# Performance work log

Hardware: AMD Instinct MI355X
Metric: run time of the kernel (lower is better)

Reference implementation:

```python
import jax, jax.numpy as jnp
import numpy as np

L_IN, L_K = 1, 1            # degree ranges (0..L)
C_IN, K_CH, H = 16, 8, 4    # in_channels, k_channels (per head), num_heads
C_OUT = H * K_CH            # 32
E, N_NODES, EMB = 32768, 4096, 64
M_IN, M_K = (L_IN + 1) ** 2, (L_K + 1) ** 2


def _so2_pairs(L_in, L_out):
    # enumerate SO(2)-equivariant weight blocks: for each order m, all (l_in, l_out)
    # pairs with l >= m; m=0 uses 1 matrix, m>0 uses 2 (real/imag parts).
    pairs, w = [], 0
    for m in range(min(L_in, L_out) + 1):
        for l_in in range(m, L_in + 1):
            for l_out in range(m, L_out + 1):
                pairs.append((m, l_in, l_out, w))
                w += 1 if m == 0 else 2
    return pairs, w

_PAIRS, NUM_W = _so2_pairs(L_IN, L_K)  # NUM_W = 6 for L_in=L_k=1


def so2_linear(x, W, L_in, L_out):
    # x: [E, (L_in+1)^2, Cin]; W: [NUM_W, Cin, Cout] (shared) or [E, NUM_W, Cin, Cout] (per-edge)
    per_edge = (W.ndim == 4)
    Cout = W.shape[-1]
    out = jnp.zeros((x.shape[0], (L_out + 1) ** 2, Cout), x.dtype)

    def mat(xs, w):
        return jnp.einsum('ec,eco->eo', xs, W[:, w]) if per_edge else xs @ W[w]

    pairs, _ = _so2_pairs(L_in, L_out)
    for m, l_in, l_out, w in pairs:
        i_in, i_out = l_in * (l_in + 1), l_out * (l_out + 1)  # flat index of (l, m=0)
        if m == 0:
            out = out.at[:, i_out].add(mat(x[:, i_in], w))
        else:
            xp, xn = x[:, i_in + m], x[:, i_in - m]
            out = out.at[:, i_out + m].add(mat(xp, w) - mat(xn, w + 1))
            out = out.at[:, i_out - m].add(mat(xp, w + 1) + mat(xn, w))
    return out


def segment_softmax(z, index, num_segments):
    # PyG-style softmax over ragged neighborhoods (max is detached, as in PyG)
    zmax = jax.lax.stop_gradient(jax.ops.segment_max(z, index, num_segments=num_segments))
    e = jnp.exp(z - zmax[index])
    denom = jax.ops.segment_sum(e, index, num_segments=num_segments)
    return e / denom[index]


def setup_inputs() -> dict:
    key = jax.random.key(0)
    ks = jax.random.split(key, 6)
    x_q = jax.random.normal(ks[0], (E, M_IN, C_IN), jnp.float32)
    x_k = jax.random.normal(ks[1], (E, M_IN, C_IN), jnp.float32)
    edge_emb = jax.random.normal(ks[2], (E, EMB), jnp.float32)
    index = jnp.sort(jax.random.randint(ks[3], (E,), 0, N_NODES))
    W_q = jax.random.normal(ks[4], (NUM_W, C_IN, C_OUT), jnp.float32) / np.sqrt(C_IN)
    W_p = jax.random.normal(ks[5], (EMB, NUM_W * C_IN * C_OUT), jnp.float32) / np.sqrt(EMB)
    return {"x_q": x_q, "x_k": x_k, "edge_emb": edge_emb, "index": index,
            "W_q": W_q, "W_p": W_p, "num_nodes": N_NODES}


def reference(x_q, x_k, edge_emb, index, W_q, W_p, num_nodes):
    # q_ij = W_Q x_i ; static SO2 weights
    q = so2_linear(x_q, W_q, L_IN, L_K).reshape(-1, M_K, H, K_CH)
    # k_ij = W_K(||r_ij||) x_j ; per-edge dynamic SO2 weights from edge embedding
    W_k = (edge_emb @ W_p).reshape(-1, NUM_W, C_IN, C_OUT)
    k = so2_linear(x_k, W_k, L_IN, L_K).reshape(-1, M_K, H, K_CH)
    scale = (K_CH // H) ** (-0.5)  # faithful to original: (k_channels // num_heads)**-0.5
    z = (q * k).sum((-1, -3)) * scale  # [E, H]
    return segment_softmax(z, index, num_nodes)
```

## Files before the change

kernel.cpp:

```cpp
#include <hip/hip_runtime.h>
#include <math.h>

#define E_TOTAL 32768
#define NUM_NODES 4096
#define SCALE 0.70710678118654752f

typedef __attribute__((ext_vector_type(8))) short bfrag;
typedef __attribute__((ext_vector_type(16))) float facc;

#define MFMA __builtin_amdgcn_mfma_f32_32x32x16_bf16

__device__ inline unsigned short f2bf(float f) {
  unsigned int u = __float_as_uint(f);
  unsigned int r = (u + 0x7FFFu + ((u >> 16) & 1u)) >> 16;
  return (unsigned short)r;
}
__device__ inline float bf2f(unsigned short s) {
  return __uint_as_float(((unsigned int)s) << 16);
}
__device__ inline void cvt8(const float* v, bfrag& hi, bfrag& lo) {
#pragma unroll
  for (int i = 0; i < 8; ++i) {
    unsigned short h = f2bf(v[i]);
    hi[i] = (short)h;
    lo[i] = (short)f2bf(v[i] - bf2f(h));
  }
}

__global__ __launch_bounds__(256) void prep_kernel(
    const float* __restrict__ Wp, const float* __restrict__ Wq,
    const int* __restrict__ index,
    unsigned short* __restrict__ fragWp, unsigned short* __restrict__ fragWq,
    int* __restrict__ offs)
{
  const int b = blockIdx.x, t = threadIdx.x;
  if (b < 96) {
    __shared__ unsigned short lds[4096];
    const int c = b / 6, w = b - c * 6;
    const int colbase = w * 512 + c * 32;
    const int cl = t & 31, dg = t >> 5;
#pragma unroll
    for (int i = 0; i < 8; ++i) {
      const int d = dg * 8 + i;
      const float v = Wp[(size_t)d * 3072 + colbase + cl];
      const unsigned short hi = f2bf(v);
      const unsigned short lo = f2bf(v - bf2f(hi));
      const int ks = d >> 4;
      const int lane = ((d >> 3) & 1) * 32 + cl;
      const int j = d & 7;
      lds[(ks * 2 + 0) * 512 + lane * 8 + j] = hi;
      lds[(ks * 2 + 1) * 512 + lane * 8 + j] = lo;
    }
    __syncthreads();
    const int wslot0 = (w == 0) ? 0 : (w == 1) ? 64 : (w == 2) ? 16
                     : (w == 3) ? 80 : (w == 4) ? 32 : 48;
    unsigned short* dst = fragWp + (size_t)(wslot0 + c) * 4096;
    ((uint4*)dst)[t] = ((const uint4*)lds)[t];
    ((uint4*)dst)[t + 256] = ((const uint4*)lds)[t + 256];
  } else if (b < 103) {
    const int slot = b - 96;
    const int w = (slot == 6) ? 5 : slot;
    const float sgn = (slot == 6) ? -1.f : 1.f;
    for (int tt = t; tt < 512; tt += 256) {
      const int lane = tt >> 3, j = tt & 7;
      const int o = lane & 31, c = (lane >> 5) * 8 + j;
      const float v = sgn * Wq[(size_t)(w * 16 + c) * 32 + o];
      const unsigned short hi = f2bf(v);
      const unsigned short lo = f2bf(v - bf2f(hi));
      fragWq[slot * 1024 + lane * 8 + j] = hi;
      fragWq[slot * 1024 + 512 + lane * 8 + j] = lo;
    }
  } else {
    const int tg = (b - 103) * 256 + t;
    if (tg >= E_TOTAL) return;
    const int cur = index[tg];
    const int prev = (tg == 0) ? -1 : index[tg - 1];
    for (int n = prev + 1; n <= cur; ++n) offs[n] = tg;
    if (tg == E_TOTAL - 1)
      for (int n = cur + 1; n <= NUM_NODES; ++n) offs[n] = E_TOTAL;
  }
}

__global__ __launch_bounds__(256, 1) void main_kernel(
    const float* __restrict__ x_q, const float* __restrict__ x_k,
    const float* __restrict__ emb,
    const unsigned short* __restrict__ fragWp,
    const unsigned short* __restrict__ fragWq,
    float* __restrict__ z)
{
  __shared__ float xk_t[64][129];
  __shared__ float zred[4][64][4];

  const int t = threadIdx.x;
  const int lane = t & 63, wv = t >> 6;
  const int pr = wv & 1, pairI = wv >> 1;
  const int col = lane & 31, half = lane >> 5;
  const int eb = blockIdx.x * 128;
  const int el0 = pairI * 64 + col;
  const int el1 = el0 + 32;
  const int e0 = eb + el0, e1 = eb + el1;

  {
    const int er = t & 127, dh = (t >> 7) * 32;
    const float* src = x_k + (size_t)(eb + er) * 64 + dh;
#pragma unroll
    for (int i = 0; i < 8; ++i) {
      float4 v = *(const float4*)(src + i * 4);
      xk_t[dh + i * 4 + 0][er] = v.x;
      xk_t[dh + i * 4 + 1][er] = v.y;
      xk_t[dh + i * 4 + 2][er] = v.z;
      xk_t[dh + i * 4 + 3][er] = v.w;
    }
  }

  bfrag ebh0[4], ebl0[4], ebh1[4], ebl1[4];
#pragma unroll
  for (int ks = 0; ks < 4; ++ks) {
    float tmp[8];
    *(float4*)&tmp[0] = *(const float4*)(emb + (size_t)e0 * 64 + ks * 16 + half * 8);
    *(float4*)&tmp[4] = *(const float4*)(emb + (size_t)e0 * 64 + ks * 16 + half * 8 + 4);
    cvt8(tmp, ebh0[ks], ebl0[ks]);
    *(float4*)&tmp[0] = *(const float4*)(emb + (size_t)e1 * 64 + ks * 16 + half * 8);
    *(float4*)&tmp[4] = *(const float4*)(emb + (size_t)e1 * 64 + ks * 16 + half * 8 + 4);
    cvt8(tmp, ebh1[ks], ebl1[ks]);
  }

  facc kaP0 = {0}, kaQ0 = {0}, kaP1 = {0}, kaQ1 = {0};

  __syncthreads();

  const unsigned short* fb = fragWp + lane * 8;
  const int qb0 = (pr ? 64 : 0) * 4096;
  const int qb1 = (pr ? 80 : 16) * 4096;
  const int qb2 = 32 * 4096;
  const int qb3 = 48 * 4096;
  const int r2 = pr ? 48 : 16;
  const int r3 = pr ? 16 : 48;
  const float sg3 = pr ? -1.f : 1.f;

#define TILE(WB, XA, XB, KA, KB)                                              \
  {                                                                           \
    const unsigned short* wb_ = (WB);                                         \
    bfrag fh[4], fl[4];                                                       \
    _Pragma("unroll")                                                         \
    for (int ks = 0; ks < 4; ++ks) {                                          \
      *(uint4*)&fh[ks] = *(const uint4*)(wb_ + ks * 1024);                    \
      *(uint4*)&fl[ks] = *(const uint4*)(wb_ + ks * 1024 + 512);              \
    }                                                                         \
    facc cc = {0.f}, cd = {0.f};                                              \
    _Pragma("unroll")                                                         \
    for (int ks = 0; ks < 4; ++ks) {                                          \
      cc = MFMA(fh[ks], ebh0[ks], cc, 0, 0, 0);                               \
      cd = MFMA(fh[ks], ebh1[ks], cd, 0, 0, 0);                               \
      cc = MFMA(fh[ks], ebl0[ks], cc, 0, 0, 0);                               \
      cd = MFMA(fh[ks], ebl1[ks], cd, 0, 0, 0);                               \
      cc = MFMA(fl[ks], ebh0[ks], cc, 0, 0, 0);                               \
      cd = MFMA(fl[ks], ebh1[ks], cd, 0, 0, 0);                               \
    }                                                                         \
    _Pragma("unroll")                                                         \
    for (int r = 0; r < 16; ++r) {                                            \
      (KA)[r] = fmaf((XA), cc[r], (KA)[r]);                                   \
      (KB)[r] = fmaf((XB), cd[r], (KB)[r]);                                   \
    }                                                                         \
  }

  for (int c = 0; c < 16; ++c) {
    const float xs0a = xk_t[c][el0],          xs0b = xk_t[c][el1];
    const float xs1a = xk_t[32 + c][el0],     xs1b = xk_t[32 + c][el1];
    const float xs2a = xk_t[r2 + c][el0],     xs2b = xk_t[r2 + c][el1];
    const float xs3a = sg3 * xk_t[r3 + c][el0], xs3b = sg3 * xk_t[r3 + c][el1];
    TILE(fb + qb0 + c * 4096, xs0a, xs0b, kaP0, kaP1)
    TILE(fb + qb1 + c * 4096, xs1a, xs1b, kaP0, kaP1)
    TILE(fb + qb2 + c * 4096, xs2a, xs2b, kaQ0, kaQ1)
    TILE(fb + qb3 + c * 4096, xs3a, xs3b, kaQ0, kaQ1)
  }
#undef TILE

#define QTERM(QA_, A_, S_)                                                    \
  {                                                                           \
    bfrag wh, wl;                                                             \
    *(uint4*)&wh = *(const uint4*)(fragWq + (S_)*1024 + lane * 8);            \
    *(uint4*)&wl = *(const uint4*)(fragWq + (S_)*1024 + 512 + lane * 8);      \
    QA_ = MFMA(wh, xqh[A_], QA_, 0, 0, 0);                                    \
    QA_ = MFMA(wh, xql[A_], QA_, 0, 0, 0);                                    \
    QA_ = MFMA(wl, xqh[A_], QA_, 0, 0, 0);                                    \
  }

#pragma unroll
  for (int blk = 0; blk < 2; ++blk) {
    const int e = blk ? e1 : e0;
    bfrag xqh[4], xql[4];
#pragma unroll
    for (int a = 0; a < 4; ++a) {
      float tmp[8];
      *(float4*)&tmp[0] = *(const float4*)(x_q + (size_t)e * 64 + a * 16 + half * 8);
      *(float4*)&tmp[4] = *(const float4*)(x_q + (size_t)e * 64 + a * 16 + half * 8 + 4);
      cvt8(tmp, xqh[a], xql[a]);
    }
    facc qaP = {0.f}, qaQ = {0.f};
    if (pr == 0) {
      QTERM(qaP, 0, 0) QTERM(qaP, 2, 2)
      QTERM(qaQ, 1, 4) QTERM(qaQ, 3, 5)
    } else {
      QTERM(qaP, 0, 1) QTERM(qaP, 2, 3)
      QTERM(qaQ, 3, 4) QTERM(qaQ, 1, 6)
    }
    const facc& kp = blk ? kaP1 : kaP0;
    const facc& kq = blk ? kaQ1 : kaQ0;
    float zp0 = 0.f, zp1 = 0.f, zp2 = 0.f, zp3 = 0.f;
#pragma unroll
    for (int r = 0; r < 16; ++r) {
      const float v = qaP[r] * kp[r] + qaQ[r] * kq[r];
      if (r < 4) zp0 += v;
      else if (r < 8) zp1 += v;
      else if (r < 12) zp2 += v;
      else zp3 += v;
    }
    zp0 += __shfl_xor(zp0, 32);
    zp1 += __shfl_xor(zp1, 32);
    zp2 += __shfl_xor(zp2, 32);
    zp3 += __shfl_xor(zp3, 32);
    if (half == 0) {
      float4 v = {zp0, zp1, zp2, zp3};
      *(float4*)&zred[wv][blk * 32 + col][0] = v;
    }
  }
#undef QTERM

  __syncthreads();
  if (pr == 0 && half == 0) {
#pragma unroll
    for (int blk = 0; blk < 2; ++blk) {
      const int idx = blk * 32 + col;
      float4 a = *(const float4*)&zred[wv][idx][0];
      float4 b = *(const float4*)&zred[wv ^ 1][idx][0];
      float4 o = {(a.x + b.x) * SCALE, (a.y + b.y) * SCALE,
                  (a.z + b.z) * SCALE, (a.w + b.w) * SCALE};
      *(float4*)&z[(size_t)(eb + pairI * 64 + idx) * 4] = o;
    }
  }
}

__global__ __launch_bounds__(256) void softmax_kernel(
    const float* __restrict__ z, const int* __restrict__ offs,
    float* __restrict__ out)
{
  const int node = blockIdx.x * 4 + (threadIdx.x >> 6);
  const int lane = threadIdx.x & 63;
  const int start = offs[node], end = offs[node + 1];
  if (start >= end) return;
  const int h = lane & 3, eo = lane >> 2;
  float m = -INFINITY;
  for (int e = start + eo; e < end; e += 16) m = fmaxf(m, z[(size_t)e * 4 + h]);
#pragma unroll
  for (int s = 4; s < 64; s <<= 1) m = fmaxf(m, __shfl_xor(m, s));
  float sum = 0.f;
  for (int e = start + eo; e < end; e += 16) sum += __expf(z[(size_t)e * 4 + h] - m);
#pragma unroll
  for (int s = 4; s < 64; s <<= 1) sum += __shfl_xor(sum, s);
  const float inv = 1.f / sum;
  for (int e = start + eo; e < end; e += 16)
    out[(size_t)e * 4 + h] = __expf(z[(size_t)e * 4 + h] - m) * inv;
}

extern "C" void kernel_launch(void* const* d_in, const int* in_sizes, int n_in,
                              void* d_out, int out_size, void* d_ws, size_t ws_size,
                              hipStream_t stream) {
  const float* x_q = (const float*)d_in[0];
  const float* x_k = (const float*)d_in[1];
  const float* emb = (const float*)d_in[2];
  const int* index = (const int*)d_in[3];
  const float* W_q = (const float*)d_in[4];
  const float* W_p = (const float*)d_in[5];
  float* out = (float*)d_out;

  char* ws = (char*)d_ws;
  float* z = (float*)ws;
  int* offs = (int*)(ws + 524288);
  unsigned short* fragWp = (unsigned short*)(ws + 524288 + 32768);
  unsigned short* fragWq = (unsigned short*)(ws + 524288 + 32768 + 786432);

  prep_kernel<<<231, 256, 0, stream>>>(W_p, W_q, index, fragWp, fragWq, offs);
  main_kernel<<<256, 256, 0, stream>>>(x_q, x_k, emb, fragWp, fragWq, z);
  softmax_kernel<<<1024, 256, 0, stream>>>(z, offs, out);
}
```

Measured before the change: 134.4 us.

## Split input-channel loop across two wave groups with 8-wave blocks

Doubles the main kernel's block to 512 threads and gives each wave pair half of the 16 input channels in the per-edge SO(2) key accumulation. The four partial z contributions are summed through a larger shared reduction buffer. The aim is more resident waves per CU, so MFMA and load latency are better hidden, since the grid of 256 blocks leaves one small block per CU. In exchange, the q-projection and embedding-fragment loads are repeated in both halves. The tighter launch bound (512, 2) caps registers per thread and may cause spills.

```diff
diff --git a/kernel.cpp b/kernel.cpp
--- a/kernel.cpp
+++ b/kernel.cpp
@@ -81,7 +81,7 @@
   }
 }
 
-__global__ __launch_bounds__(256, 1) void main_kernel(
+__global__ __launch_bounds__(512, 2) void main_kernel(
     const float* __restrict__ x_q, const float* __restrict__ x_k,
     const float* __restrict__ emb,
     const unsigned short* __restrict__ fragWp,
@@ -89,11 +89,11 @@
     float* __restrict__ z)
 {
   __shared__ float xk_t[64][129];
-  __shared__ float zred[4][64][4];
+  __shared__ float zred[8][64][4];
 
   const int t = threadIdx.x;
   const int lane = t & 63, wv = t >> 6;
-  const int pr = wv & 1, pairI = wv >> 1;
+  const int pairI = wv >> 2, chalf = (wv >> 1) & 1, pr = wv & 1;
   const int col = lane & 31, half = lane >> 5;
   const int eb = blockIdx.x * 128;
   const int el0 = pairI * 64 + col;
@@ -101,15 +101,15 @@
   const int e0 = eb + el0, e1 = eb + el1;
 
   {
-    const int er = t & 127, dh = (t >> 7) * 32;
-    const float* src = x_k + (size_t)(eb + er) * 64 + dh;
-#pragma unroll
-    for (int i = 0; i < 8; ++i) {
+    const int er = t & 127, dq = (t >> 7) * 16;
+    const float* src = x_k + (size_t)(eb + er) * 64 + dq;
+#pragma unroll
+    for (int i = 0; i < 4; ++i) {
       float4 v = *(const float4*)(src + i * 4);
-      xk_t[dh + i * 4 + 0][er] = v.x;
-      xk_t[dh + i * 4 + 1][er] = v.y;
-      xk_t[dh + i * 4 + 2][er] = v.z;
-      xk_t[dh + i * 4 + 3][er] = v.w;
+      xk_t[dq + i * 4 + 0][er] = v.x;
+      xk_t[dq + i * 4 + 1][er] = v.y;
+      xk_t[dq + i * 4 + 2][er] = v.z;
+      xk_t[dq + i * 4 + 3][er] = v.w;
     }
   }
 
@@ -164,15 +164,16 @@
     }                                                                         \
   }
 
-  for (int c = 0; c < 16; ++c) {
-    const float xs0a = xk_t[c][el0],          xs0b = xk_t[c][el1];
-    const float xs1a = xk_t[32 + c][el0],     xs1b = xk_t[32 + c][el1];
-    const float xs2a = xk_t[r2 + c][el0],     xs2b = xk_t[r2 + c][el1];
-    const float xs3a = sg3 * xk_t[r3 + c][el0], xs3b = sg3 * xk_t[r3 + c][el1];
-    TILE(fb + qb0 + c * 4096, xs0a, xs0b, kaP0, kaP1)
-    TILE(fb + qb1 + c * 4096, xs1a, xs1b, kaP0, kaP1)
-    TILE(fb + qb2 + c * 4096, xs2a, xs2b, kaQ0, kaQ1)
-    TILE(fb + qb3 + c * 4096, xs3a, xs3b, kaQ0, kaQ1)
+  for (int c = 0; c < 8; ++c) {
+    const int cg = chalf * 8 + c;
+    const float xs0a = xk_t[cg][el0],           xs0b = xk_t[cg][el1];
+    const float xs1a = xk_t[32 + cg][el0],      xs1b = xk_t[32 + cg][el1];
+    const float xs2a = xk_t[r2 + cg][el0],      xs2b = xk_t[r2 + cg][el1];
+    const float xs3a = sg3 * xk_t[r3 + cg][el0], xs3b = sg3 * xk_t[r3 + cg][el1];
+    TILE(fb + qb0 + cg * 4096, xs0a, xs0b, kaP0, kaP1)
+    TILE(fb + qb1 + cg * 4096, xs1a, xs1b, kaP0, kaP1)
+    TILE(fb + qb2 + cg * 4096, xs2a, xs2b, kaQ0, kaQ1)
+    TILE(fb + qb3 + cg * 4096, xs3a, xs3b, kaQ0, kaQ1)
   }
 #undef TILE
 
@@ -228,14 +229,18 @@
 #undef QTERM
 
   __syncthreads();
-  if (pr == 0 && half == 0) {
+  if (pr == 0 && chalf == 0 && half == 0) {
 #pragma unroll
     for (int blk = 0; blk < 2; ++blk) {
       const int idx = blk * 32 + col;
-      float4 a = *(const float4*)&zred[wv][idx][0];
-      float4 b = *(const float4*)&zred[wv ^ 1][idx][0];
-      float4 o = {(a.x + b.x) * SCALE, (a.y + b.y) * SCALE,
-                  (a.z + b.z) * SCALE, (a.w + b.w) * SCALE};
+      float4 a = *(const float4*)&zred[wv + 0][idx][0];
+      float4 b = *(const float4*)&zred[wv + 1][idx][0];
+      float4 cc = *(const float4*)&zred[wv + 2][idx][0];
+      float4 d = *(const float4*)&zred[wv + 3][idx][0];
+      float4 o = {(a.x + b.x + cc.x + d.x) * SCALE,
+                  (a.y + b.y + cc.y + d.y) * SCALE,
+                  (a.z + b.z + cc.z + d.z) * SCALE,
+                  (a.w + b.w + cc.w + d.w) * SCALE};
       *(float4*)&z[(size_t)(eb + pairI * 64 + idx) * 4] = o;
     }
   }
@@ -281,6 +286,6 @@
   unsigned short* fragWq = (unsigned short*)(ws + 524288 + 32768 + 786432);
 
   prep_kernel<<<231, 256, 0, stream>>>(W_p, W_q, index, fragWp, fragWq, offs);
-  main_kernel<<<256, 256, 0, stream>>>(x_q, x_k, emb, fragWp, fragWq, z);
+  main_kernel<<<256, 512, 0, stream>>>(x_q, x_k, emb, fragWp, fragWq, z);
   softmax_kernel<<<1024, 256, 0, stream>>>(z, offs, out);
 }
```

Result: slower. 175.7 us (+30.6%).
